# Optimization experiments

Measured on AMD Instinct MI355X. Metric: run time of the kernel, lower is better.

Reference implementation:

```python
import jax, jax.numpy as jnp
import numpy as np

EPS = 1e-5
KERNELS = [3, 3, 5, 7]  # 2*i+1 for i>=1, first layer k=3


def _conv_relu_bn(x, w, b, gamma, beta, rmean, rvar):
    # x: [B, Cin, S], w: [Cout, Cin, K]
    k = w.shape[-1]
    y = jax.lax.conv_general_dilated(
        x, w, window_strides=(1,), padding=[(k // 2, k // 2)],
        dimension_numbers=("NCW", "OIW", "NCW"))
    y = y + b[None, :, None]
    y = jax.nn.relu(y)
    # BatchNorm1d in inference mode (running stats)
    inv = gamma[None, :, None] / jnp.sqrt(rvar[None, :, None] + EPS)
    return (y - rmean[None, :, None]) * inv + beta[None, :, None]


def setup_inputs() -> dict:
    key = jax.random.key(0)
    ks = jax.random.split(key, 32)
    B, S = 128, 8192
    inp = {"x": jax.random.normal(ks[0], (B, 4, S), dtype=jnp.float32)}
    cin = 4
    for i, k in enumerate(KERNELS):
        inp[f"w{i}"] = jax.random.normal(ks[1 + i], (32, cin, k), dtype=jnp.float32) * 0.1
        inp[f"b{i}"] = jnp.zeros((32,), jnp.float32)
        inp[f"g{i}"] = jnp.ones((32,), jnp.float32)   # BN gamma
        inp[f"bb{i}"] = jnp.zeros((32,), jnp.float32)  # BN beta
        inp[f"rm{i}"] = jnp.zeros((32,), jnp.float32)  # running mean
        inp[f"rv{i}"] = jnp.ones((32,), jnp.float32)   # running var
        cin = 32
    inp["fw1"] = jax.random.normal(ks[10], (16, 32), dtype=jnp.float32) * 0.1
    inp["fb1"] = jnp.zeros((16,), jnp.float32)
    inp["fw2"] = jax.random.normal(ks[11], (1, 16), dtype=jnp.float32) * 0.1
    inp["fb2"] = jnp.zeros((1,), jnp.float32)
    return inp


def reference(x,
              w0, b0, g0, bb0, rm0, rv0,
              w1, b1, g1, bb1, rm1, rv1,
              w2, b2, g2, bb2, rm2, rv2,
              w3, b3, g3, bb3, rm3, rv3,
              fw1, fb1, fw2, fb2):
    x = _conv_relu_bn(x, w0, b0, g0, bb0, rm0, rv0)
    x = _conv_relu_bn(x, w1, b1, g1, bb1, rm1, rv1)
    x = _conv_relu_bn(x, w2, b2, g2, bb2, rm2, rv2)
    x = _conv_relu_bn(x, w3, b3, g3, bb3, rm3, rv3)
    # [B, 32, S] -> [B, S, 32]; the original per-timestep MLP loop is one batched GEMM
    h = jnp.einsum("bcs,hc->bsh", x, fw1) + fb1
    h = jax.nn.relu(h)  # Dropout(0.1) is identity in eval
    out = jnp.einsum("bsh,oh->bso", h, fw2) + fb2
    return out[..., 0]  # squeeze(-1) -> [B, S]
```

## Files before the change

kernel.cpp:

```cpp
#include <hip/hip_runtime.h>

#define SEQ    8192
#define NPOS   256
#define S_TILE 244
#define NROWS  264
#define CSH    (NROWS*16)
#define NTHR   256
#define NREC   33
#define BN_HALFOFF (NREC*512)

typedef __attribute__((ext_vector_type(8)))  _Float16 half8;
typedef __attribute__((ext_vector_type(4)))  _Float16 half4v;
typedef __attribute__((ext_vector_type(16))) float    f32x16;

__device__ __forceinline__ int uni(int v){ return __builtin_amdgcn_readfirstlane(v); }

template<int K>
__device__ __forceinline__ float fold_bias(const float* __restrict__ W, int co,
    const float* __restrict__ gp, const float* __restrict__ bbp,
    const float* __restrict__ rmp, const float* __restrict__ rvp)
{
    float acc = 0.f;
#pragma unroll
    for (int ci = 0; ci < 32; ++ci) {
        float sp = gp[ci] * rsqrtf(rvp[ci] + 1e-5f);
        float tp = bbp[ci] - rmp[ci]*sp;
        float wsum = 0.f;
#pragma unroll
        for (int tap = 0; tap < K; ++tap) wsum += W[(co*32 + ci)*K + tap];
        acc += wsum * tp;
    }
    return acc;
}

extern "C" __global__ void prep_kernel(
    const float* w0, const float* w1, const float* w2, const float* w3,
    const float* b0, const float* g0, const float* bb0, const float* rm0, const float* rv0,
    const float* b1, const float* g1, const float* bb1, const float* rm1, const float* rv1,
    const float* b2, const float* g2, const float* bb2, const float* rm2, const float* rv2,
    const float* b3, const float* g3, const float* bb3, const float* rm3, const float* rv3,
    const float* fw1, const float* fb1, _Float16* ws)
{
    const int tid = threadIdx.x;
    const int rec = blockIdx.x;
    if (rec < NREC) {
        if (tid < 64) {
            const int lane = tid, co = lane & 31, hi = lane >> 5;
            half8 h;
            if (rec == 0) {
#pragma unroll
                for (int j = 0; j < 8; ++j) {
                    int k = hi*8 + j;
                    float wv = 0.f;
                    if (k < 12) wv = w0[(co*4 + (k & 3))*3 + (k >> 2)];
                    h[j] = (_Float16)wv;
                }
            } else if (rec < 31) {
                const float* W; const float *gp, *rvp; int K, r2;
                if      (rec < 7)  { W = w1; K = 3; r2 = rec - 1;  gp = g0; rvp = rv0; }
                else if (rec < 17) { W = w2; K = 5; r2 = rec - 7;  gp = g1; rvp = rv1; }
                else               { W = w3; K = 7; r2 = rec - 17; gp = g2; rvp = rv2; }
                const int tap = r2 >> 1, cib = r2 & 1;
#pragma unroll
                for (int j = 0; j < 8; ++j) {
                    int ci = cib*16 + hi*8 + j;
                    float s = gp[ci] * rsqrtf(rvp[ci] + 1e-5f);
                    h[j] = (_Float16)(W[(co*32 + ci)*K + tap] * s);
                }
            } else {
                const int cib = rec - 31;
#pragma unroll
                for (int j = 0; j < 8; ++j) {
                    int ci = cib*16 + hi*8 + j;
                    float s = g3[ci] * rsqrtf(rv3[ci] + 1e-5f);
                    h[j] = (_Float16)((co < 16) ? fw1[co*32 + ci]*s : 0.f);
                }
            }
            *(half8*)(ws + rec*512 + lane*8) = h;
        }
    } else {
        float* fa = (float*)(ws + BN_HALFOFF);
        if (tid < 128) {
            int l = tid >> 5, co = tid & 31;
            const float *g, *bb, *rm, *rv, *bi;
            if      (l == 0) { g=g0; bb=bb0; rm=rm0; rv=rv0; bi=b0; }
            else if (l == 1) { g=g1; bb=bb1; rm=rm1; rv=rv1; bi=b1; }
            else if (l == 2) { g=g2; bb=bb2; rm=rm2; rv=rv2; bi=b2; }
            else             { g=g3; bb=bb3; rm=rm3; rv=rv3; bi=b3; }
            float s = g[co] * rsqrtf(rv[co] + 1e-5f);
            float t = bb[co] - rm[co]*s;
            float bias = bi[co];
            if      (l == 1) bias += fold_bias<3>(w1, co, g0, bb0, rm0, rv0);
            else if (l == 2) bias += fold_bias<5>(w2, co, g1, bb1, rm1, rv1);
            else if (l == 3) bias += fold_bias<7>(w3, co, g2, bb2, rm2, rv2);
            fa[(l*32 + co)*2 + 0] = bias;
            fa[(l*32 + co)*2 + 1] = -t / s;
        } else if (tid < 144) {
            int hh = tid - 128;
            float acc = fb1[hh];
#pragma unroll
            for (int c = 0; c < 32; ++c) {
                float s3 = g3[c] * rsqrtf(rv3[c] + 1e-5f);
                float t3 = bb3[c] - rm3[c]*s3;
                acc += fw1[hh*32 + c] * t3;
            }
            fa[256 + hh] = acc;
        }
    }
}

__device__ __forceinline__ void conv_epi(
    f32x16* acc, const float2* __restrict__ bo,
    _Float16* outb, int s0, int doff, int P0, int n, int hi)
{
    float2 pv[16];
#pragma unroll
    for (int g = 0; g < 4; ++g)
#pragma unroll
        for (int i = 0; i < 4; ++i) pv[g*4 + i] = bo[g*8 + 4*hi + i];

#pragma unroll
    for (int t = 0; t < 2; ++t) {
        const int pos = P0 + t*32 + n;
        const bool oob = (unsigned)(s0 + doff + pos) >= SEQ;
#pragma unroll
        for (int g = 0; g < 4; ++g) {
            half4v hv;
#pragma unroll
            for (int i = 0; i < 4; ++i) {
                const float2 p = pv[g*4 + i];
                const float v = fmaxf(acc[t][g*4 + i] + p.x, 0.f);
                hv[i] = (_Float16)(oob ? p.y : v);
            }
            *(half4v*)(outb + (g >> 1)*CSH + pos*16 + (g & 1)*8 + hi*4) = hv;
        }
    }
}

template<int K, int DOFF>
__device__ __forceinline__ void conv32(
    const _Float16* __restrict__ rec, const float2* __restrict__ bo,
    const _Float16* in, _Float16* outb, int s0, int P0, int lane)
{
    const int n = lane & 31, hi = lane >> 5;
    const _Float16* bbase = in + (P0 + n)*16 + hi*8;

    f32x16 acc[2];
#pragma unroll
    for (int t = 0; t < 2; ++t)
#pragma unroll
        for (int i = 0; i < 16; ++i) acc[t][i] = 0.f;

#pragma unroll
    for (int tap = 0; tap < K; ++tap) {
        half8 a0 = *(const half8*)(rec + (tap*2 + 0)*512 + lane*8);
        half8 a1 = *(const half8*)(rec + (tap*2 + 1)*512 + lane*8);
#pragma unroll
        for (int t = 0; t < 2; ++t) {
            half8 b0 = *(const half8*)(bbase + 0*CSH + (t*32 + tap)*16);
            half8 b1 = *(const half8*)(bbase + 1*CSH + (t*32 + tap)*16);
            acc[t] = __builtin_amdgcn_mfma_f32_32x32x16_f16(a0, b0, acc[t], 0, 0, 0);
            acc[t] = __builtin_amdgcn_mfma_f32_32x32x16_f16(a1, b1, acc[t], 0, 0, 0);
        }
    }
    conv_epi(acc, bo, outb, s0, DOFF, P0, n, hi);
}

__device__ __forceinline__ void conv32L0(
    const _Float16* __restrict__ rec, const float2* __restrict__ bo,
    const _Float16* in, _Float16* outb, int s0, int P0, int lane)
{
    const int n = lane & 31, hi = lane >> 5;
    half8 a = *(const half8*)(rec + lane*8);
    f32x16 acc[2];
#pragma unroll
    for (int t = 0; t < 2; ++t)
#pragma unroll
        for (int i = 0; i < 16; ++i) acc[t][i] = 0.f;
#pragma unroll
    for (int t = 0; t < 2; ++t) {
        half8 b = *(const half8*)(in + (P0 + t*32 + n)*16 + hi*8);
        acc[t] = __builtin_amdgcn_mfma_f32_32x32x16_f16(a, b, acc[t], 0, 0, 0);
    }
    conv_epi(acc, bo, outb, s0, -6, P0, n, hi);
}

extern "C" __global__ void __launch_bounds__(NTHR, 4)
dnashape_mfma(const float* __restrict__ x, const _Float16* __restrict__ ws,
              const float* __restrict__ fw2, const float* __restrict__ fb2,
              float* __restrict__ out)
{
    __shared__ _Float16 bufA[2*CSH] __attribute__((aligned(16)));
    __shared__ _Float16 bufB[2*CSH] __attribute__((aligned(16)));

    const int tid = threadIdx.x;
    const int s0  = blockIdx.x * S_TILE;
    const int b   = blockIdx.y;

    {
        const float* xb = x + b*4*SEQ;
        const int r  = tid;
        const int sb = s0 - 7 + r;
        _Float16 h[16];
#pragma unroll
        for (int tap = 0; tap < 3; ++tap) {
            const int sg = sb + tap;
            const bool ok = (unsigned)sg < SEQ;
#pragma unroll
            for (int ci = 0; ci < 4; ++ci)
                h[tap*4 + ci] = (_Float16)(ok ? xb[ci*SEQ + sg] : 0.f);
        }
#pragma unroll
        for (int j = 12; j < 16; ++j) h[j] = (_Float16)0.f;
        *(half8*)(bufB + r*16)     = *(half8*)(h);
        *(half8*)(bufB + r*16 + 8) = *(half8*)(h + 8);
        if (tid < 64) {
            const half8 z = {0,0,0,0,0,0,0,0};
            _Float16* base = (tid & 32) ? bufA : bufB;
            *(half8*)(base + ((tid >> 4) & 1)*CSH + 256*16 + (tid & 15)*8) = z;
        }
    }
    __syncthreads();

    const int lane = tid & 63;
    const int wv   = uni(tid >> 6);
    const int P0   = wv * 64;
    const float*  fa = (const float*)(ws + BN_HALFOFF);
    const float2* bo = (const float2*)fa;

    conv32L0     (ws,           bo,      bufB, bufA, s0, P0, lane);
    __syncthreads();
    conv32<3, -5>(ws + 1*512,   bo + 32, bufA, bufB, s0, P0, lane);
    __syncthreads();
    conv32<5, -3>(ws + 7*512,   bo + 64, bufB, bufA, s0, P0, lane);
    __syncthreads();
    conv32<7,  0>(ws + 17*512,  bo + 96, bufA, bufB, s0, P0, lane);
    __syncthreads();

    {
        const int n = lane & 31, hi = lane >> 5;
        half8 am0 = *(const half8*)(ws + 31*512 + lane*8);
        half8 am1 = *(const half8*)(ws + 32*512 + lane*8);
        float fb1v[8], fw2v[8];
#pragma unroll
        for (int r = 0; r < 8; ++r) {
            const int co = (r & 3) + 8*(r >> 2) + 4*hi;
            fb1v[r] = fa[256 + co];
            fw2v[r] = fw2[co];
        }
        const float fb2v = fb2[0];
#pragma unroll
        for (int t = 0; t < 2; ++t) {
            const int pos = P0 + t*32 + n;
            half8 bf0 = *(const half8*)(bufB + 0*CSH + pos*16 + hi*8);
            half8 bf1 = *(const half8*)(bufB + 1*CSH + pos*16 + hi*8);
            f32x16 d;
#pragma unroll
            for (int i = 0; i < 16; ++i) d[i] = 0.f;
            d = __builtin_amdgcn_mfma_f32_32x32x16_f16(am0, bf0, d, 0, 0, 0);
            d = __builtin_amdgcn_mfma_f32_32x32x16_f16(am1, bf1, d, 0, 0, 0);
            float part = 0.f;
#pragma unroll
            for (int r = 0; r < 8; ++r)
                part += fmaxf(d[r] + fb1v[r], 0.f) * fw2v[r];
            part += __shfl_xor(part, 32, 64);
            const int gpos = s0 + pos;
            if (hi == 0 && pos < S_TILE && gpos < SEQ)
                out[b*SEQ + gpos] = part + fb2v;
        }
    }
}

extern "C" void kernel_launch(void* const* d_in, const int* in_sizes, int n_in,
                              void* d_out, int out_size, void* d_ws, size_t ws_size,
                              hipStream_t stream) {
    const float* p[29];
    for (int i = 0; i < 29; ++i) p[i] = (const float*)d_in[i];
    _Float16* ws = (_Float16*)d_ws;

    prep_kernel<<<dim3(NREC + 1), 144, 0, stream>>>(
        p[1], p[7], p[13], p[19],
        p[2], p[3], p[4], p[5], p[6],
        p[8], p[9], p[10], p[11], p[12],
        p[14], p[15], p[16], p[17], p[18],
        p[20], p[21], p[22], p[23], p[24],
        p[25], p[26], ws);

    dim3 grid((SEQ + S_TILE - 1) / S_TILE, 128);
    dnashape_mfma<<<grid, NTHR, 0, stream>>>(p[0], (const _Float16*)ws,
                                             p[27], p[28], (float*)d_out);
}
```

Before: 171.2 us.

## Shrink LDS tiles, widen epilogue stores via permlane swap, raise occupancy

Drops the padding rows so each channel-half buffer is exactly 256 rows, which reduces LDS per block and lets the launch bound ask for five blocks per CU instead of four. The epilogue now packs fp16 pairs and uses v_permlane32_swap to exchange halves between lane groups, so each lane issues one 16-byte LDS store instead of several 8-byte ones. Bias and OOB-fill loads are hoisted ahead of the MFMA loop. The risk is that halo reads past row 255 now land in the neighbouring buffer's data rather than in zeroed padding; this only stays correct if those edge outputs are discarded. A tighter register budget may also cause spills.

```diff
diff --git a/kernel.cpp b/kernel.cpp
--- a/kernel.cpp
+++ b/kernel.cpp
@@ -3,17 +3,22 @@
 #define SEQ    8192
 #define NPOS   256
 #define S_TILE 244
-#define NROWS  264
-#define CSH    (NROWS*16)
+#define CSH    4096
 #define NTHR   256
 #define NREC   33
 #define BN_HALFOFF (NREC*512)
 
 typedef __attribute__((ext_vector_type(8)))  _Float16 half8;
-typedef __attribute__((ext_vector_type(4)))  _Float16 half4v;
 typedef __attribute__((ext_vector_type(16))) float    f32x16;
+typedef unsigned int u32;
+typedef __attribute__((ext_vector_type(4))) u32 u32x4;
 
 __device__ __forceinline__ int uni(int v){ return __builtin_amdgcn_readfirstlane(v); }
+
+__device__ __forceinline__ u32 pkh2(float a, float b){
+    union { _Float16 h[2]; u32 u; } v;
+    v.h[0] = (_Float16)a; v.h[1] = (_Float16)b; return v.u;
+}
 
 template<int K>
 __device__ __forceinline__ float fold_bias(const float* __restrict__ W, int co,
@@ -110,29 +115,34 @@
 }
 
 __device__ __forceinline__ void conv_epi(
-    f32x16* acc, const float2* __restrict__ bo,
+    f32x16* acc, const float2* pv,
     _Float16* outb, int s0, int doff, int P0, int n, int hi)
 {
-    float2 pv[16];
-#pragma unroll
-    for (int g = 0; g < 4; ++g)
-#pragma unroll
-        for (int i = 0; i < 4; ++i) pv[g*4 + i] = bo[g*8 + 4*hi + i];
-
 #pragma unroll
     for (int t = 0; t < 2; ++t) {
         const int pos = P0 + t*32 + n;
         const bool oob = (unsigned)(s0 + doff + pos) >= SEQ;
-#pragma unroll
-        for (int g = 0; g < 4; ++g) {
-            half4v hv;
+        u32 P[4][2];
+#pragma unroll
+        for (int q = 0; q < 4; ++q) {
+            float v[4];
 #pragma unroll
             for (int i = 0; i < 4; ++i) {
-                const float2 p = pv[g*4 + i];
-                const float v = fmaxf(acc[t][g*4 + i] + p.x, 0.f);
-                hv[i] = (_Float16)(oob ? p.y : v);
+                const float2 p = pv[q*4 + i];
+                float r = fmaxf(acc[t][q*4 + i] + p.x, 0.f);
+                v[i] = oob ? p.y : r;
             }
-            *(half4v*)(outb + (g >> 1)*CSH + pos*16 + (g & 1)*8 + hi*4) = hv;
+            P[q][0] = pkh2(v[0], v[1]);
+            P[q][1] = pkh2(v[2], v[3]);
+        }
+#pragma unroll
+        for (int c = 0; c < 2; ++c) {
+            u32 a0 = P[2*c][0], b0 = P[2*c+1][0];
+            u32 a1 = P[2*c][1], b1 = P[2*c+1][1];
+            asm("v_permlane32_swap_b32 %0, %1" : "+v"(a0), "+v"(b0));
+            asm("v_permlane32_swap_b32 %0, %1" : "+v"(a1), "+v"(b1));
+            u32x4 w = {a0, a1, b0, b1};
+            *(u32x4*)(outb + c*CSH + pos*16 + hi*8) = w;
         }
     }
 }
@@ -144,6 +154,12 @@
 {
     const int n = lane & 31, hi = lane >> 5;
     const _Float16* bbase = in + (P0 + n)*16 + hi*8;
+
+    float2 pv[16];
+#pragma unroll
+    for (int q = 0; q < 4; ++q)
+#pragma unroll
+        for (int i = 0; i < 4; ++i) pv[q*4 + i] = bo[q*8 + 4*hi + i];
 
     f32x16 acc[2];
 #pragma unroll
@@ -163,7 +179,7 @@
             acc[t] = __builtin_amdgcn_mfma_f32_32x32x16_f16(a1, b1, acc[t], 0, 0, 0);
         }
     }
-    conv_epi(acc, bo, outb, s0, DOFF, P0, n, hi);
+    conv_epi(acc, pv, outb, s0, DOFF, P0, n, hi);
 }
 
 __device__ __forceinline__ void conv32L0(
@@ -171,6 +187,12 @@
     const _Float16* in, _Float16* outb, int s0, int P0, int lane)
 {
     const int n = lane & 31, hi = lane >> 5;
+    float2 pv[16];
+#pragma unroll
+    for (int q = 0; q < 4; ++q)
+#pragma unroll
+        for (int i = 0; i < 4; ++i) pv[q*4 + i] = bo[q*8 + 4*hi + i];
+
     half8 a = *(const half8*)(rec + lane*8);
     f32x16 acc[2];
 #pragma unroll
@@ -182,16 +204,17 @@
         half8 b = *(const half8*)(in + (P0 + t*32 + n)*16 + hi*8);
         acc[t] = __builtin_amdgcn_mfma_f32_32x32x16_f16(a, b, acc[t], 0, 0, 0);
     }
-    conv_epi(acc, bo, outb, s0, -6, P0, n, hi);
-}
-
-extern "C" __global__ void __launch_bounds__(NTHR, 4)
+    conv_epi(acc, pv, outb, s0, -6, P0, n, hi);
+}
+
+extern "C" __global__ void __launch_bounds__(NTHR, 5)
 dnashape_mfma(const float* __restrict__ x, const _Float16* __restrict__ ws,
               const float* __restrict__ fw2, const float* __restrict__ fb2,
               float* __restrict__ out)
 {
-    __shared__ _Float16 bufA[2*CSH] __attribute__((aligned(16)));
-    __shared__ _Float16 bufB[2*CSH] __attribute__((aligned(16)));
+    __shared__ _Float16 lds[4*CSH] __attribute__((aligned(16)));
+    _Float16* bufA = lds;
+    _Float16* bufB = lds + 2*CSH;
 
     const int tid = threadIdx.x;
     const int s0  = blockIdx.x * S_TILE;
@@ -214,11 +237,6 @@
         for (int j = 12; j < 16; ++j) h[j] = (_Float16)0.f;
         *(half8*)(bufB + r*16)     = *(half8*)(h);
         *(half8*)(bufB + r*16 + 8) = *(half8*)(h + 8);
-        if (tid < 64) {
-            const half8 z = {0,0,0,0,0,0,0,0};
-            _Float16* base = (tid & 32) ? bufA : bufB;
-            *(half8*)(base + ((tid >> 4) & 1)*CSH + 256*16 + (tid & 15)*8) = z;
-        }
     }
     __syncthreads();
 
```

After: 180.9 us. +5.6%, slower.
